# Kernel tuning notes

Hardware: AMD Instinct MI355X
Metric: run time of the kernel (lower is better)

Reference implementation:

```python
import jax, jax.numpy as jnp
import numpy as np

B, S, H, C = 16, 4096, 1024, 64

def setup_inputs() -> dict:
    key = jax.random.key(0)
    k1, k2 = jax.random.split(key)
    hidden = jax.random.normal(k1, (B, S, H), dtype=jnp.float32)
    querys = jax.random.normal(k2, (C, H), dtype=jnp.float32)
    return {"hidden": hidden, "querys": querys}

def reference(hidden, querys):
    # scores: [B, C, S] = einsum over hidden_size
    scores = jnp.einsum('bsh,ch->bcs', hidden, querys)
    # softmax over the sequence axis
    factor = jax.nn.softmax(scores, axis=2)
    # pooled: [B, C, H]
    result = jnp.einsum('bcs,bsh->bch', factor, hidden)
    # flatten to [B, C*H]
    return result.reshape(-1, querys.shape[0] * querys.shape[1])
```

## Files before the change

### kernel.cpp

```cpp
#include <hip/hip_runtime.h>
#include <math.h>

#define BB 16
#define SS 4096
#define HH 1024
#define CC 64

typedef __attribute__((ext_vector_type(4))) float f32x4;
typedef __attribute__((ext_vector_type(8))) short s16x8;
typedef __attribute__((ext_vector_type(4))) unsigned int u32x4;

__device__ __forceinline__ ushort f2bf(float x) {
    union { float f; unsigned u; } un; un.f = x;
    unsigned r = (un.u + 0x7FFFu + ((un.u >> 16) & 1u)) >> 16;
    return (ushort)r;
}
__device__ __forceinline__ float bf2f(ushort h) {
    union { unsigned u; float f; } un; un.u = ((unsigned)h) << 16; return un.f;
}

__device__ __forceinline__ unsigned hipack(unsigned v1, unsigned v0) {
    return __builtin_amdgcn_perm(v1, v0, 0x07060302u);
}

__device__ __forceinline__ void cvt8(f32x4 f0, f32x4 f1, s16x8& hi, s16x8& lo) {
    u32x4 u0 = __builtin_bit_cast(u32x4, f0);
    u32x4 u1 = __builtin_bit_cast(u32x4, f1);
    u32x4 b0 = u0 + 0x8000u;
    u32x4 b1 = u1 + 0x8000u;
    f32x4 m0 = __builtin_bit_cast(f32x4, b0 & 0xFFFF0000u);
    f32x4 m1 = __builtin_bit_cast(f32x4, b1 & 0xFFFF0000u);
    u32x4 r0 = __builtin_bit_cast(u32x4, f0 - m0);
    u32x4 r1 = __builtin_bit_cast(u32x4, f1 - m1);
    u32x4 h = { hipack(b0.y, b0.x), hipack(b0.w, b0.z),
                hipack(b1.y, b1.x), hipack(b1.w, b1.z) };
    u32x4 l = { hipack(r0.y, r0.x), hipack(r0.w, r0.z),
                hipack(r1.y, r1.x), hipack(r1.w, r1.z) };
    hi = __builtin_bit_cast(s16x8, h);
    lo = __builtin_bit_cast(s16x8, l);
}

__global__ __launch_bounds__(256) void prep_querys_kernel(
    const float* __restrict__ q, ushort* __restrict__ qhi, ushort* __restrict__ qlo)
{
    const int i4 = blockIdx.x * 256 + threadIdx.x;
    const float4 v = ((const float4*)q)[i4];
    ushort4 h, l;
    h.x = f2bf(v.x); l.x = f2bf(v.x - bf2f(h.x));
    h.y = f2bf(v.y); l.y = f2bf(v.y - bf2f(h.y));
    h.z = f2bf(v.z); l.z = f2bf(v.z - bf2f(h.z));
    h.w = f2bf(v.w); l.w = f2bf(v.w - bf2f(h.w));
    ((ushort4*)qhi)[i4] = h;
    ((ushort4*)qlo)[i4] = l;
}

__global__ __launch_bounds__(256) void scores_kernel(
    const float* __restrict__ hidden, const ushort* __restrict__ qhi,
    const ushort* __restrict__ qlo, float* __restrict__ scores,
    ushort* __restrict__ hid_hi)
{
    const int b  = blockIdx.y;
    const int s0 = blockIdx.x * 128;
    const int t  = threadIdx.x;
    const int w = t >> 6, lane = t & 63, col = lane & 15, quad = lane >> 4;

    const int r0 = s0 + w * 32 + col;
    const int r1 = r0 + 16;
    const float* a0p = hidden + ((size_t)b * SS + r0) * HH + quad * 8;
    const float* a1p = hidden + ((size_t)b * SS + r1) * HH + quad * 8;
    ushort* h0p = hid_hi + ((size_t)b * SS + r0) * HH + quad * 8;
    ushort* h1p = hid_hi + ((size_t)b * SS + r1) * HH + quad * 8;
    const ushort* qbh = qhi + (size_t)col * HH + quad * 8;
    const ushort* qbl = qlo + (size_t)col * HH + quad * 8;

    f32x4 acc[2][4];
#pragma unroll
    for (int i = 0; i < 2; ++i)
#pragma unroll
        for (int j = 0; j < 4; ++j) acc[i][j] = (f32x4){0.f, 0.f, 0.f, 0.f};

    f32x4 Aa0, Aa1, Aa2, Aa3, Ab0, Ab1, Ab2, Ab3;

#define LOADA(P0, P1, P2, P3, K) do { \
    P0 = *(const f32x4*)(a0p + (K));     P1 = *(const f32x4*)(a0p + (K) + 4); \
    P2 = *(const f32x4*)(a1p + (K));     P3 = *(const f32x4*)(a1p + (K) + 4); } while (0)

#define SCOMP(P0, P1, P2, P3, K) do { \
    s16x8 ah0, al0, ah1, al1; \
    cvt8(P0, P1, ah0, al0); \
    cvt8(P2, P3, ah1, al1); \
    *(s16x8*)(h0p + (K)) = ah0; \
    *(s16x8*)(h1p + (K)) = ah1; \
    _Pragma("unroll") \
    for (int nt = 0; nt < 4; ++nt) { \
        const s16x8 bh = *(const s16x8*)(qbh + nt * 16 * HH + (K)); \
        const s16x8 bl = *(const s16x8*)(qbl + nt * 16 * HH + (K)); \
        acc[0][nt] = __builtin_amdgcn_mfma_f32_16x16x32_bf16(ah0, bh, acc[0][nt], 0, 0, 0); \
        acc[0][nt] = __builtin_amdgcn_mfma_f32_16x16x32_bf16(ah0, bl, acc[0][nt], 0, 0, 0); \
        acc[0][nt] = __builtin_amdgcn_mfma_f32_16x16x32_bf16(al0, bh, acc[0][nt], 0, 0, 0); \
        acc[1][nt] = __builtin_amdgcn_mfma_f32_16x16x32_bf16(ah1, bh, acc[1][nt], 0, 0, 0); \
        acc[1][nt] = __builtin_amdgcn_mfma_f32_16x16x32_bf16(ah1, bl, acc[1][nt], 0, 0, 0); \
        acc[1][nt] = __builtin_amdgcn_mfma_f32_16x16x32_bf16(al1, bh, acc[1][nt], 0, 0, 0); \
    } } while (0)

    LOADA(Aa0, Aa1, Aa2, Aa3, 0);
    for (int k0 = 0; k0 < HH; k0 += 64) {
        LOADA(Ab0, Ab1, Ab2, Ab3, k0 + 32);
        SCOMP(Aa0, Aa1, Aa2, Aa3, k0);
        if (k0 + 64 < HH) LOADA(Aa0, Aa1, Aa2, Aa3, k0 + 64);
        SCOMP(Ab0, Ab1, Ab2, Ab3, k0 + 32);
    }
#undef LOADA
#undef SCOMP

#pragma unroll
    for (int mt = 0; mt < 2; ++mt)
#pragma unroll
        for (int nt = 0; nt < 4; ++nt) {
            const int c = nt * 16 + col;
            const int s = s0 + w * 32 + mt * 16 + quad * 4;
            *(f32x4*)&scores[((size_t)(b * CC + c)) * SS + s] = acc[mt][nt];
        }
}

__global__ __launch_bounds__(256) void softmax_kernel(
    const float* __restrict__ scores, ushort* __restrict__ factor)
{
    const float* p = scores + (size_t)blockIdx.x * SS;
    ushort* f = factor + (size_t)blockIdx.x * SS;
    const int t = threadIdx.x;
    float4 v[4];
    float m = -3.0e38f;
#pragma unroll
    for (int i = 0; i < 4; ++i) {
        v[i] = *(const float4*)&p[t * 4 + i * 1024];
        m = fmaxf(m, fmaxf(fmaxf(v[i].x, v[i].y), fmaxf(v[i].z, v[i].w)));
    }
#pragma unroll
    for (int off = 1; off < 64; off <<= 1) m = fmaxf(m, __shfl_xor(m, off));
    __shared__ float redm[4];
    __shared__ float reds[4];
    const int wave = t >> 6, lane = t & 63;
    if (lane == 0) redm[wave] = m;
    __syncthreads();
    m = fmaxf(fmaxf(redm[0], redm[1]), fmaxf(redm[2], redm[3]));

    float sum = 0.0f;
#pragma unroll
    for (int i = 0; i < 4; ++i) {
        v[i].x = __expf(v[i].x - m); v[i].y = __expf(v[i].y - m);
        v[i].z = __expf(v[i].z - m); v[i].w = __expf(v[i].w - m);
        sum += (v[i].x + v[i].y) + (v[i].z + v[i].w);
    }
#pragma unroll
    for (int off = 1; off < 64; off <<= 1) sum += __shfl_xor(sum, off);
    if (lane == 0) reds[wave] = sum;
    __syncthreads();
    sum = (reds[0] + reds[1]) + (reds[2] + reds[3]);
    const float inv = 1.0f / sum;
#pragma unroll
    for (int i = 0; i < 4; ++i) {
        ushort4 o;
        o.x = f2bf(v[i].x * inv); o.y = f2bf(v[i].y * inv);
        o.z = f2bf(v[i].z * inv); o.w = f2bf(v[i].w * inv);
        ((ushort4*)f)[t + i * 256] = o;
    }
}

__global__ __launch_bounds__(256) void pool_kernel(
    const ushort* __restrict__ hid_hi, const ushort* __restrict__ factor,
    float* __restrict__ parts)
{
    const int b  = blockIdx.y;
    const int h0 = blockIdx.x * 64;
    const int ks = blockIdx.z;
    const int sbeg = ks * (SS / 4);
    const int t = threadIdx.x;
    const int w = t >> 6, lane = t & 63, col = lane & 15, quad = lane >> 4;

    f32x4 acc[4];
#pragma unroll
    for (int j = 0; j < 4; ++j) acc[j] = (f32x4){0.f, 0.f, 0.f, 0.f};

    const ushort* fptr = factor + ((size_t)(b * CC + w * 16 + col)) * SS + sbeg + quad * 8;
    const ushort* hp = hid_hi + ((size_t)b * SS + sbeg + quad * 8) * HH + h0 + col;

    ushort ra[4][8], rb[4][8];
    s16x8 faA, faB;

#define PLOAD(R, FA, SC) do { \
    FA = *(const s16x8*)(fptr + (SC)); \
    _Pragma("unroll") for (int nt = 0; nt < 4; ++nt) \
    _Pragma("unroll") for (int j = 0; j < 8; ++j) \
        R[nt][j] = hp[(size_t)((SC) + j) * HH + nt * 16]; } while (0)

#define PCOMP(R, FA) do { \
    _Pragma("unroll") for (int nt = 0; nt < 4; ++nt) { \
        u32x4 d = { (unsigned)R[nt][0] | ((unsigned)R[nt][1] << 16), \
                    (unsigned)R[nt][2] | ((unsigned)R[nt][3] << 16), \
                    (unsigned)R[nt][4] | ((unsigned)R[nt][5] << 16), \
                    (unsigned)R[nt][6] | ((unsigned)R[nt][7] << 16) }; \
        const s16x8 hb = __builtin_bit_cast(s16x8, d); \
        acc[nt] = __builtin_amdgcn_mfma_f32_16x16x32_bf16(FA, hb, acc[nt], 0, 0, 0); \
    } } while (0)

    PLOAD(ra, faA, 0);
    for (int sc = 0; sc < SS / 4; sc += 64) {
        PLOAD(rb, faB, sc + 32);
        PCOMP(ra, faA);
        if (sc + 64 < SS / 4) PLOAD(ra, faA, sc + 64);
        PCOMP(rb, faB);
    }
#undef PLOAD
#undef PCOMP

    float* dst = parts + (size_t)ks * (BB * CC * HH) + (size_t)b * (CC * HH);
#pragma unroll
    for (int nt = 0; nt < 4; ++nt) {
        const int h = h0 + nt * 16 + col;
#pragma unroll
        for (int r = 0; r < 4; ++r) {
            const int c = w * 16 + quad * 4 + r;
            dst[(size_t)c * HH + h] = acc[nt][r];
        }
    }
}

__global__ __launch_bounds__(256) void reduce4_kernel(
    const float* __restrict__ parts, float* __restrict__ out)
{
    const int i = blockIdx.x * 256 + threadIdx.x;
    const float4* p = (const float4*)parts;
    const float4 a = p[i];
    const float4 b = p[i + 262144];
    const float4 c = p[i + 524288];
    const float4 d = p[i + 786432];
    float4 r;
    r.x = (a.x + b.x) + (c.x + d.x);
    r.y = (a.y + b.y) + (c.y + d.y);
    r.z = (a.z + b.z) + (c.z + d.z);
    r.w = (a.w + b.w) + (c.w + d.w);
    ((float4*)out)[i] = r;
}

extern "C" void kernel_launch(void* const* d_in, const int* in_sizes, int n_in,
                              void* d_out, int out_size, void* d_ws, size_t ws_size,
                              hipStream_t stream)
{
    const float* hidden = (const float*)d_in[0];
    const float* querys = (const float*)d_in[1];
    float* out = (float*)d_out;

    float*  scores = (float*)d_ws;
    float*  parts  = (float*)d_ws;
    ushort* factor = (ushort*)((char*)d_ws + (16u << 20));
    ushort* qhi    = (ushort*)((char*)d_ws + (24u << 20));
    ushort* qlo    = qhi + CC * HH;
    ushort* hid_hi = (ushort*)((char*)d_ws + (32u << 20));

    prep_querys_kernel<<<dim3(CC * HH / 1024), 256, 0, stream>>>(querys, qhi, qlo);
    scores_kernel<<<dim3(SS / 128, BB), 256, 0, stream>>>(hidden, qhi, qlo, scores, hid_hi);
    softmax_kernel<<<dim3(BB * CC), 256, 0, stream>>>(scores, factor);
    pool_kernel<<<dim3(HH / 64, BB, 4), 256, 0, stream>>>(hid_hi, factor, parts);
    reduce4_kernel<<<dim3(1024), 256, 0, stream>>>(parts, out);
}
```

Measured before the change: 526.2 us.

## Shrink per-block tiles in scores and pool kernels to raise parallelism

The scores kernel now handles 32 sequence rows per block and splits the 64 query columns across wave pairs, so each wave owns a 16x32 tile instead of 32x64. Only one wave pair writes the bf16 copy of hidden. The pool kernel's H tile drops from 64 to 32 columns, doubling the grid. The aim is more blocks and lower register pressure for better occupancy and latency hiding. The cost is that each hidden row is now loaded from global memory by two waves, and per-wave reuse of loaded data is lower.

```diff
diff --git a/kernel.cpp b/kernel.cpp
--- a/kernel.cpp
+++ b/kernel.cpp
@@ -60,67 +60,57 @@
     ushort* __restrict__ hid_hi)
 {
     const int b  = blockIdx.y;
-    const int s0 = blockIdx.x * 128;
+    const int s0 = blockIdx.x * 32;
     const int t  = threadIdx.x;
     const int w = t >> 6, lane = t & 63, col = lane & 15, quad = lane >> 4;
-
-    const int r0 = s0 + w * 32 + col;
-    const int r1 = r0 + 16;
+    const int rg = w & 1;
+    const int ch = w >> 1;
+
+    const int r0 = s0 + rg * 16 + col;
     const float* a0p = hidden + ((size_t)b * SS + r0) * HH + quad * 8;
-    const float* a1p = hidden + ((size_t)b * SS + r1) * HH + quad * 8;
     ushort* h0p = hid_hi + ((size_t)b * SS + r0) * HH + quad * 8;
-    ushort* h1p = hid_hi + ((size_t)b * SS + r1) * HH + quad * 8;
-    const ushort* qbh = qhi + (size_t)col * HH + quad * 8;
-    const ushort* qbl = qlo + (size_t)col * HH + quad * 8;
-
-    f32x4 acc[2][4];
-#pragma unroll
-    for (int i = 0; i < 2; ++i)
-#pragma unroll
-        for (int j = 0; j < 4; ++j) acc[i][j] = (f32x4){0.f, 0.f, 0.f, 0.f};
-
-    f32x4 Aa0, Aa1, Aa2, Aa3, Ab0, Ab1, Ab2, Ab3;
-
-#define LOADA(P0, P1, P2, P3, K) do { \
-    P0 = *(const f32x4*)(a0p + (K));     P1 = *(const f32x4*)(a0p + (K) + 4); \
-    P2 = *(const f32x4*)(a1p + (K));     P3 = *(const f32x4*)(a1p + (K) + 4); } while (0)
-
-#define SCOMP(P0, P1, P2, P3, K) do { \
-    s16x8 ah0, al0, ah1, al1; \
+    const ushort* qbh = qhi + (size_t)(ch * 32 + col) * HH + quad * 8;
+    const ushort* qbl = qlo + (size_t)(ch * 32 + col) * HH + quad * 8;
+
+    f32x4 acc[2];
+    acc[0] = (f32x4){0.f, 0.f, 0.f, 0.f};
+    acc[1] = (f32x4){0.f, 0.f, 0.f, 0.f};
+
+    f32x4 Aa0, Aa1, Ab0, Ab1;
+
+#define LOADA(P0, P1, K) do { \
+    P0 = *(const f32x4*)(a0p + (K)); \
+    P1 = *(const f32x4*)(a0p + (K) + 4); } while (0)
+
+#define SCOMP(P0, P1, K) do { \
+    s16x8 ah0, al0; \
     cvt8(P0, P1, ah0, al0); \
-    cvt8(P2, P3, ah1, al1); \
-    *(s16x8*)(h0p + (K)) = ah0; \
-    *(s16x8*)(h1p + (K)) = ah1; \
+    if (ch == 0) *(s16x8*)(h0p + (K)) = ah0; \
     _Pragma("unroll") \
-    for (int nt = 0; nt < 4; ++nt) { \
+    for (int nt = 0; nt < 2; ++nt) { \
         const s16x8 bh = *(const s16x8*)(qbh + nt * 16 * HH + (K)); \
         const s16x8 bl = *(const s16x8*)(qbl + nt * 16 * HH + (K)); \
-        acc[0][nt] = __builtin_amdgcn_mfma_f32_16x16x32_bf16(ah0, bh, acc[0][nt], 0, 0, 0); \
-        acc[0][nt] = __builtin_amdgcn_mfma_f32_16x16x32_bf16(ah0, bl, acc[0][nt], 0, 0, 0); \
-        acc[0][nt] = __builtin_amdgcn_mfma_f32_16x16x32_bf16(al0, bh, acc[0][nt], 0, 0, 0); \
-        acc[1][nt] = __builtin_amdgcn_mfma_f32_16x16x32_bf16(ah1, bh, acc[1][nt], 0, 0, 0); \
-        acc[1][nt] = __builtin_amdgcn_mfma_f32_16x16x32_bf16(ah1, bl, acc[1][nt], 0, 0, 0); \
-        acc[1][nt] = __builtin_amdgcn_mfma_f32_16x16x32_bf16(al1, bh, acc[1][nt], 0, 0, 0); \
+        acc[nt] = __builtin_amdgcn_mfma_f32_16x16x32_bf16(ah0, bh, acc[nt], 0, 0, 0); \
+        acc[nt] = __builtin_amdgcn_mfma_f32_16x16x32_bf16(ah0, bl, acc[nt], 0, 0, 0); \
+        acc[nt] = __builtin_amdgcn_mfma_f32_16x16x32_bf16(al0, bh, acc[nt], 0, 0, 0); \
     } } while (0)
 
-    LOADA(Aa0, Aa1, Aa2, Aa3, 0);
+    LOADA(Aa0, Aa1, 0);
     for (int k0 = 0; k0 < HH; k0 += 64) {
-        LOADA(Ab0, Ab1, Ab2, Ab3, k0 + 32);
-        SCOMP(Aa0, Aa1, Aa2, Aa3, k0);
-        if (k0 + 64 < HH) LOADA(Aa0, Aa1, Aa2, Aa3, k0 + 64);
-        SCOMP(Ab0, Ab1, Ab2, Ab3, k0 + 32);
+        LOADA(Ab0, Ab1, k0 + 32);
+        SCOMP(Aa0, Aa1, k0);
+        if (k0 + 64 < HH) LOADA(Aa0, Aa1, k0 + 64);
+        SCOMP(Ab0, Ab1, k0 + 32);
     }
 #undef LOADA
 #undef SCOMP
 
 #pragma unroll
-    for (int mt = 0; mt < 2; ++mt)
-#pragma unroll
-        for (int nt = 0; nt < 4; ++nt) {
-            const int c = nt * 16 + col;
-            const int s = s0 + w * 32 + mt * 16 + quad * 4;
-            *(f32x4*)&scores[((size_t)(b * CC + c)) * SS + s] = acc[mt][nt];
-        }
+    for (int nt = 0; nt < 2; ++nt) {
+        const int c = ch * 32 + nt * 16 + col;
+        const int s = s0 + rg * 16 + quad * 4;
+        *(f32x4*)&scores[((size_t)(b * CC + c)) * SS + s] = acc[nt];
+    }
 }
 
 __global__ __launch_bounds__(256) void softmax_kernel(
@@ -172,30 +162,30 @@
     float* __restrict__ parts)
 {
     const int b  = blockIdx.y;
-    const int h0 = blockIdx.x * 64;
+    const int h0 = blockIdx.x * 32;
     const int ks = blockIdx.z;
     const int sbeg = ks * (SS / 4);
     const int t = threadIdx.x;
     const int w = t >> 6, lane = t & 63, col = lane & 15, quad = lane >> 4;
 
-    f32x4 acc[4];
-#pragma unroll
-    for (int j = 0; j < 4; ++j) acc[j] = (f32x4){0.f, 0.f, 0.f, 0.f};
+    f32x4 acc[2];
+    acc[0] = (f32x4){0.f, 0.f, 0.f, 0.f};
+    acc[1] = (f32x4){0.f, 0.f, 0.f, 0.f};
 
     const ushort* fptr = factor + ((size_t)(b * CC + w * 16 + col)) * SS + sbeg + quad * 8;
     const ushort* hp = hid_hi + ((size_t)b * SS + sbeg + quad * 8) * HH + h0 + col;
 
-    ushort ra[4][8], rb[4][8];
+    ushort ra[2][8], rb[2][8];
     s16x8 faA, faB;
 
 #define PLOAD(R, FA, SC) do { \
     FA = *(const s16x8*)(fptr + (SC)); \
-    _Pragma("unroll") for (int nt = 0; nt < 4; ++nt) \
+    _Pragma("unroll") for (int nt = 0; nt < 2; ++nt) \
     _Pragma("unroll") for (int j = 0; j < 8; ++j) \
         R[nt][j] = hp[(size_t)((SC) + j) * HH + nt * 16]; } while (0)
 
 #define PCOMP(R, FA) do { \
-    _Pragma("unroll") for (int nt = 0; nt < 4; ++nt) { \
+    _Pragma("unroll") for (int nt = 0; nt < 2; ++nt) { \
         u32x4 d = { (unsigned)R[nt][0] | ((unsigned)R[nt][1] << 16), \
                     (unsigned)R[nt][2] | ((unsigned)R[nt][3] << 16), \
                     (unsigned)R[nt][4] | ((unsigned)R[nt][5] << 16), \
@@ -216,7 +206,7 @@
 
     float* dst = parts + (size_t)ks * (BB * CC * HH) + (size_t)b * (CC * HH);
 #pragma unroll
-    for (int nt = 0; nt < 4; ++nt) {
+    for (int nt = 0; nt < 2; ++nt) {
         const int h = h0 + nt * 16 + col;
 #pragma unroll
         for (int r = 0; r < 4; ++r) {
@@ -259,8 +249,8 @@
     ushort* hid_hi = (ushort*)((char*)d_ws + (32u << 20));
 
     prep_querys_kernel<<<dim3(CC * HH / 1024), 256, 0, stream>>>(querys, qhi, qlo);
-    scores_kernel<<<dim3(SS / 128, BB), 256, 0, stream>>>(hidden, qhi, qlo, scores, hid_hi);
+    scores_kernel<<<dim3(SS / 32, BB), 256, 0, stream>>>(hidden, qhi, qlo, scores, hid_hi);
     softmax_kernel<<<dim3(BB * CC), 256, 0, stream>>>(scores, factor);
-    pool_kernel<<<dim3(HH / 64, BB, 4), 256, 0, stream>>>(hid_hi, factor, parts);
+    pool_kernel<<<dim3(HH / 32, BB, 4), 256, 0, stream>>>(hid_hi, factor, parts);
     reduce4_kernel<<<dim3(1024), 256, 0, stream>>>(parts, out);
 }
```

Measured after the change: 650.5 us. 1.24x slower.
